# Optimization experiments

Hardware: AMD Instinct MI355X
Metric: run time of the kernel (lower is better)

## Reference

```python
import jax, jax.numpy as jnp
import numpy as np

NUM_PROJS = 8
BLOCK = 128      # key_block_size; with n=4096 -> 32 blocks, query_block_size=128 too
SAMPLE = 128     # sample_size
HEAD_DIM = 64
SCALE = HEAD_DIM ** -0.5

def _gray_perm(n):
    # AngularLSH._unit_hamming_distance_array: Gray-code ordering of 2^n sign buckets
    a = np.array([0, 1], dtype=np.int32)
    for _ in range(n - 1):
        a = np.concatenate([a, a[::-1] + a.shape[0]])
    return a

PERM = jnp.asarray(_gray_perm(NUM_PROJS))
ENC = jnp.asarray(2 ** np.arange(NUM_PROJS), dtype=jnp.int32)

def _lsh_hash(x, proj_dir):
    # x: [b,h,n,d], proj_dir: [d,r] -> Gray-coded bucket id [b,h,n]
    bits = (jnp.einsum('bhnd,dr->bhnr', x, proj_dir) > 0).astype(jnp.int32)
    return PERM[jnp.sum(bits * ENC, axis=-1)]

def _gather_seq(x, idx):
    # gather along seq axis (axis=2); idx: [b,h,m]
    return jnp.take_along_axis(x, idx[..., None], axis=2)

def _hyper_attention(q, k, v, proj_dir, sampled_set):
    # q,k,v: [b,h,n,d]; non-causal HyperAttention (n >= min_seq_len path)
    b, h, n, d = q.shape
    # --- 1. sortLSH block-diagonal attention ---
    q_idx = jnp.argsort(_lsh_hash(q, proj_dir), axis=2, stable=True)
    k_idx = jnp.argsort(_lsh_hash(k, proj_dir), axis=2, stable=True)
    q_idx_inv = jnp.argsort(q_idx, axis=2, stable=True)
    qs = _gather_seq(q, q_idx)
    ks = _gather_seq(k, k_idx)
    vs = _gather_seq(v, k_idx)
    nb = n // BLOCK
    qb = qs.reshape(b, h, nb, BLOCK, d)
    kb = ks.reshape(b, h, nb, BLOCK, d)
    vb = vs.reshape(b, h, nb, BLOCK, d)
    s = jnp.einsum('bhgqd,bhgkd->bhgqk', qb, kb) * SCALE
    lse_blk = jax.scipy.special.logsumexp(s, axis=-1).reshape(b, h, n)
    attn_blk = jnp.einsum('bhgqk,bhgkd->bhgqd', jax.nn.softmax(s, axis=-1), vb).reshape(b, h, n, d)
    # --- 2. uniformly sampled residual (low-rank correction) ---
    ksub = _gather_seq(ks, sampled_set)   # [b,h,m,d]
    vsub = _gather_seq(vs, sampled_set)
    row_blk = jnp.arange(n) // BLOCK       # query_block_size == BLOCK here
    mask = row_blk[None, None, :, None] == (sampled_set // BLOCK)[:, :, None, :]
    bias = jnp.where(mask, jnp.finfo(q.dtype).min, jnp.zeros((), q.dtype))
    sr = jnp.einsum('bhnd,bhmd->bhnm', qs, ksub) * SCALE + bias
    lse_res = jax.scipy.special.logsumexp(sr, axis=-1) + jnp.log(jnp.asarray(n / SAMPLE, q.dtype))
    attn_res = jnp.einsum('bhnm,bhmd->bhnd', jax.nn.softmax(sr, axis=-1), vsub)
    # --- combine the two attention estimates (add_self_attentions) ---
    lse = jnp.logaddexp(lse_blk, lse_res)
    w1 = jnp.exp(lse_blk - lse)[..., None]
    attn = w1 * attn_blk + (1.0 - w1) * attn_res
    # --- unsort rows back to original query order ---
    return _gather_seq(attn, q_idx_inv)

def setup_inputs() -> dict:
    key = jax.random.key(0)
    k1, k2, k3 = jax.random.split(key, 3)
    qkv = jax.random.normal(k1, (2, 4096, 3, 16, 64), dtype=jnp.float32)
    proj_dir = jax.random.normal(k2, (64, NUM_PROJS), dtype=jnp.float32)
    sampled_set = jax.random.randint(k3, (2, 16, SAMPLE), 0, 4096)
    return {"qkv": qkv, "proj_dir": proj_dir, "sampled_set": sampled_set}

def reference(qkv, proj_dir, sampled_set):
    # qkv: [B,S,3,H,D] -> q,k,v [B,H,S,D]
    q = jnp.transpose(qkv[:, :, 0], (0, 2, 1, 3))
    k = jnp.transpose(qkv[:, :, 1], (0, 2, 1, 3))
    v = jnp.transpose(qkv[:, :, 2], (0, 2, 1, 3))
    out = _hyper_attention(q, k, v, proj_dir, sampled_set)
    return jnp.transpose(out, (0, 2, 1, 3))  # [B,S,H,D]
```

## Files before the change

### kernel.cpp

```cpp
#include <hip/hip_runtime.h>
#include <hip/hip_bf16.h>

#define NSEQ 4096
#define DH 64
#define NBH 32
#define LOG32 3.4657359028f
#define QSCALE 0.125f

typedef unsigned short us8 __attribute__((ext_vector_type(8)));
typedef __bf16 bf16x8 __attribute__((ext_vector_type(8)));
typedef float f32x4 __attribute__((ext_vector_type(4)));

__device__ __forceinline__ unsigned short f2b(float x) {
    __bf16 h = (__bf16)x;
    return __builtin_bit_cast(unsigned short, h);
}
__device__ __forceinline__ bf16x8 cvt8(float4 a, float4 b) {
    us8 u;
    u[0] = f2b(a.x); u[1] = f2b(a.y); u[2] = f2b(a.z); u[3] = f2b(a.w);
    u[4] = f2b(b.x); u[5] = f2b(b.y); u[6] = f2b(b.z); u[7] = f2b(b.w);
    return __builtin_bit_cast(bf16x8, u);
}

__global__ __launch_bounds__(256) void hash_kernel(const float* __restrict__ qkv,
                                                   const float* __restrict__ proj,
                                                   unsigned short* __restrict__ hsh) {
    __shared__ float pdT[512];
    int tid = threadIdx.x;
    for (int j = tid; j < 512; j += 256) pdT[j] = proj[(j & 63) * 8 + (j >> 6)];
    __syncthreads();
    int j0 = blockIdx.x * 256 + tid;
    #pragma unroll
    for (int rep = 0; rep < 2; ++rep) {
        int j = j0 + rep * 131072;
        int ch = rep;
        int bh = (j >> 12) & 31;
        int i = j & 4095;
        int b = bh >> 4, h = bh & 15;
        const float4* src = (const float4*)(qkv + ((size_t)((b * NSEQ + i) * 3 + ch)) * 1024 + h * 64);
        double acc[8] = {0, 0, 0, 0, 0, 0, 0, 0};
        for (int d4 = 0; d4 < 16; ++d4) {
            float4 x = src[d4];
            double xx = x.x, xy = x.y, xz = x.z, xw = x.w;
            #pragma unroll
            for (int r = 0; r < 8; ++r) {
                const float4 p = *(const float4*)&pdT[r * 64 + d4 * 4];
                acc[r] += xx * p.x + xy * p.y + xz * p.z + xw * p.w;
            }
        }
        int c = 0;
        #pragma unroll
        for (int r = 0; r < 8; ++r)
            if (acc[r] > 0.0) c |= (1 << r);
        hsh[j] = (unsigned short)(c ^ (c >> 1));
    }
}

__global__ __launch_bounds__(1024) void sort_kernel(const unsigned short* __restrict__ hsh,
                                                    int* __restrict__ qidx,
                                                    int* __restrict__ kidx) {
    int blk = blockIdx.x;
    int pass = blk >> 5, bh = blk & 31;
    const unsigned short* src = hsh + pass * 131072 + bh * 4096;
    int* outg = (pass ? kidx : qidx) + bh * 4096;
    int tid = threadIdx.x;
    __shared__ unsigned short hl[4096];
    __shared__ int hist[64][256];
    __shared__ int base[256];
    for (int j = tid; j < 64 * 256; j += 1024) (&hist[0][0])[j] = 0;
    __syncthreads();
    for (int j = tid; j < 4096; j += 1024) {
        unsigned short v = src[j];
        hl[j] = v;
        atomicAdd(&hist[j >> 6][v], 1);
    }
    __syncthreads();
    int cnt_tot = 0;
    if (tid < 256) {
        int tot = 0;
        #pragma unroll
        for (int s = 0; s < 64; ++s) { int c = hist[s][tid]; hist[s][tid] = tot; tot += c; }
        base[tid] = tot;
        cnt_tot = tot;
    }
    __syncthreads();
    for (int off = 1; off < 256; off <<= 1) {
        int t = (tid >= off && tid < 256) ? base[tid - off] : 0;
        __syncthreads();
        if (tid >= off && tid < 256) base[tid] += t;
        __syncthreads();
    }
    int incl = 0;
    if (tid < 256) incl = base[tid];
    __syncthreads();
    if (tid < 256) base[tid] = incl - cnt_tot;
    __syncthreads();
    {
        int seg = tid >> 4, cls = tid & 15;
        for (int ii = 0; ii < 64; ++ii) {
            int i = (seg << 6) + ii;
            int q = hl[i];
            if ((q & 15) == cls) {
                int pos = base[q] + hist[seg][q];
                hist[seg][q] = hist[seg][q] + 1;
                outg[pos] = i;
            }
        }
    }
}

__global__ __launch_bounds__(512, 4) void attn_kernel(const float* __restrict__ qkv,
                                                      const int* __restrict__ sampled,
                                                      const int* __restrict__ qidx_g,
                                                      const int* __restrict__ kidx_g,
                                                      float* __restrict__ out) {
    int gb = blockIdx.x;
    int bh = gb >> 5, g = gb & 31;
    int b = bh >> 4, h = bh & 15;
    int tid = threadIdx.x;
    int w = tid >> 6, l = tid & 63;
    int l15 = l & 15, lq = l >> 4;

    __shared__ us8 KP[2048];
    __shared__ us8 VT[2048];
    __shared__ float colbias[256];
    __shared__ int qrow[128];
    __shared__ int krow[256];

    if (tid < 128) {
        qrow[tid] = qidx_g[bh * NSEQ + g * 128 + tid];
        krow[tid] = kidx_g[bh * NSEQ + g * 128 + tid];
        colbias[tid] = 0.0f;
    } else if (tid < 256) {
        int j = tid - 128;
        int sp = sampled[bh * 128 + j];
        krow[tid] = kidx_g[bh * NSEQ + sp];
        colbias[tid] = ((sp >> 7) == g) ? -1e30f : LOG32;
    }
    __syncthreads();

    int qr = qrow[w * 16 + l15];
    const float* qbase = qkv + ((size_t)((b * NSEQ + qr) * 3 + 0)) * 1024 + h * 64 + lq * 8;
    float4 qa0 = *(const float4*)(qbase);
    float4 qa1 = *(const float4*)(qbase + 4);
    float4 qb0 = *(const float4*)(qbase + 32);
    float4 qb1 = *(const float4*)(qbase + 36);

    #pragma unroll
    for (int rep = 0; rep < 2; ++rep) {
        int job = tid + rep * 512;
        int r = job >> 2, qt = job & 3;
        const float4* src = (const float4*)(qkv + ((size_t)((b * NSEQ + krow[r]) * 3 + 1)) * 1024 + h * 64 + qt * 16);
        float4 f0 = src[0], f1 = src[1], f2 = src[2], f3 = src[3];
        us8 u0 = __builtin_bit_cast(us8, cvt8(f0, f1));
        us8 u1 = __builtin_bit_cast(us8, cvt8(f2, f3));
        KP[r * 8 + ((qt * 2) ^ (r & 7))] = u0;
        KP[r * 8 + ((qt * 2 + 1) ^ (r & 7))] = u1;
    }
    {
        int key = tid >> 1, half = tid & 1;
        const float4* src = (const float4*)(qkv + ((size_t)((b * NSEQ + krow[key]) * 3 + 2)) * 1024 + h * 64 + half * 32);
        unsigned short* vt_us = (unsigned short*)VT;
        int kc8 = key >> 3, ke = key & 7;
        #pragma unroll
        for (int d4 = 0; d4 < 8; ++d4) {
            float4 f = src[d4];
            int d = half * 32 + d4 * 4;
            vt_us[(((d + 0) * 32 + (kc8 ^ ((d + 0) & 7))) << 3) + ke] = f2b(f.x);
            vt_us[(((d + 1) * 32 + (kc8 ^ ((d + 1) & 7))) << 3) + ke] = f2b(f.y);
            vt_us[(((d + 2) * 32 + (kc8 ^ ((d + 2) & 7))) << 3) + ke] = f2b(f.z);
            vt_us[(((d + 3) * 32 + (kc8 ^ ((d + 3) & 7))) << 3) + ke] = f2b(f.w);
        }
    }
    __syncthreads();

    bf16x8 a0 = cvt8(qa0, qa1);
    bf16x8 a1 = cvt8(qb0, qb1);
    f32x4 sreg[16];
    #pragma unroll
    for (int ct = 0; ct < 16; ++ct) {
        int kr = ct * 16 + l15;
        bf16x8 b0 = __builtin_bit_cast(bf16x8, KP[kr * 8 + (lq ^ (kr & 7))]);
        bf16x8 b1 = __builtin_bit_cast(bf16x8, KP[kr * 8 + ((lq + 4) ^ (kr & 7))]);
        f32x4 acc = {0.f, 0.f, 0.f, 0.f};
        acc = __builtin_amdgcn_mfma_f32_16x16x32_bf16(a0, b0, acc, 0, 0, 0);
        acc = __builtin_amdgcn_mfma_f32_16x16x32_bf16(a1, b1, acc, 0, 0, 0);
        float cb = colbias[kr];
        #pragma unroll
        for (int j = 0; j < 4; ++j) sreg[ct][j] = acc[j] * QSCALE + cb;
    }

    float m0 = -1e30f, m1 = -1e30f, m2 = -1e30f, m3 = -1e30f;
    #pragma unroll
    for (int ct = 0; ct < 16; ++ct) {
        m0 = fmaxf(m0, sreg[ct][0]); m1 = fmaxf(m1, sreg[ct][1]);
        m2 = fmaxf(m2, sreg[ct][2]); m3 = fmaxf(m3, sreg[ct][3]);
    }
    #pragma unroll
    for (int mask = 1; mask < 16; mask <<= 1) {
        m0 = fmaxf(m0, __shfl_xor(m0, mask));
        m1 = fmaxf(m1, __shfl_xor(m1, mask));
        m2 = fmaxf(m2, __shfl_xor(m2, mask));
        m3 = fmaxf(m3, __shfl_xor(m3, mask));
    }
    float s0 = 0.f, s1 = 0.f, s2 = 0.f, s3 = 0.f;
    #pragma unroll
    for (int ct = 0; ct < 16; ++ct) {
        float p0 = __expf(sreg[ct][0] - m0); sreg[ct][0] = p0; s0 += p0;
        float p1 = __expf(sreg[ct][1] - m1); sreg[ct][1] = p1; s1 += p1;
        float p2 = __expf(sreg[ct][2] - m2); sreg[ct][2] = p2; s2 += p2;
        float p3 = __expf(sreg[ct][3] - m3); sreg[ct][3] = p3; s3 += p3;
    }
    #pragma unroll
    for (int mask = 1; mask < 16; mask <<= 1) {
        s0 += __shfl_xor(s0, mask);
        s1 += __shfl_xor(s1, mask);
        s2 += __shfl_xor(s2, mask);
        s3 += __shfl_xor(s3, mask);
    }
    float rs0 = 1.f / s0, rs1 = 1.f / s1, rs2 = 1.f / s2, rs3 = 1.f / s3;

    __syncthreads();

    unsigned short* pp = (unsigned short*)KP;
    int wrow0 = w * 16 + lq * 4;
    #pragma unroll
    for (int ct = 0; ct < 8; ++ct) {
        int c8 = 2 * ct + (l15 >> 3), ce = l15 & 7;
        #pragma unroll
        for (int j = 0; j < 4; ++j) {
            int row = wrow0 + j;
            pp[((row * 16 + (c8 ^ (row & 7))) << 3) + ce] = f2b(sreg[ct][j]);
        }
    }
    __syncthreads();

    f32x4 oacc[4] = {{0.f,0.f,0.f,0.f},{0.f,0.f,0.f,0.f},{0.f,0.f,0.f,0.f},{0.f,0.f,0.f,0.f}};
    int prow = w * 16 + l15;
    #pragma unroll
    for (int ks = 0; ks < 4; ++ks) {
        bf16x8 pa = __builtin_bit_cast(bf16x8, KP[prow * 16 + ((ks * 4 + lq) ^ (prow & 7))]);
        #pragma unroll
        for (int ct = 0; ct < 4; ++ct) {
            int d = ct * 16 + l15;
            bf16x8 vb = __builtin_bit_cast(bf16x8, VT[d * 32 + ((ks * 4 + lq) ^ (d & 7))]);
            oacc[ct] = __builtin_amdgcn_mfma_f32_16x16x32_bf16(pa, vb, oacc[ct], 0, 0, 0);
        }
    }
    __syncthreads();
    #pragma unroll
    for (int ct = 8; ct < 16; ++ct) {
        int c8 = 2 * (ct - 8) + (l15 >> 3), ce = l15 & 7;
        #pragma unroll
        for (int j = 0; j < 4; ++j) {
            int row = wrow0 + j;
            pp[((row * 16 + (c8 ^ (row & 7))) << 3) + ce] = f2b(sreg[ct][j]);
        }
    }
    __syncthreads();
    #pragma unroll
    for (int ks = 4; ks < 8; ++ks) {
        bf16x8 pa = __builtin_bit_cast(bf16x8, KP[prow * 16 + (((ks - 4) * 4 + lq) ^ (prow & 7))]);
        #pragma unroll
        for (int ct = 0; ct < 4; ++ct) {
            int d = ct * 16 + l15;
            bf16x8 vb = __builtin_bit_cast(bf16x8, VT[d * 32 + ((ks * 4 + lq) ^ (d & 7))]);
            oacc[ct] = __builtin_amdgcn_mfma_f32_16x16x32_bf16(pa, vb, oacc[ct], 0, 0, 0);
        }
    }

    float rs[4] = {rs0, rs1, rs2, rs3};
    #pragma unroll
    for (int j = 0; j < 4; ++j) {
        int row = wrow0 + j;
        size_t obase = ((size_t)((b * NSEQ + qrow[row]) * 16 + h)) * 64;
        #pragma unroll
        for (int ct = 0; ct < 4; ++ct)
            out[obase + ct * 16 + l15] = oacc[ct][j] * rs[j];
    }
}

extern "C" void kernel_launch(void* const* d_in, const int* in_sizes, int n_in,
                              void* d_out, int out_size, void* d_ws, size_t ws_size,
                              hipStream_t stream) {
    const float* qkv = (const float*)d_in[0];
    const float* proj = (const float*)d_in[1];
    const int* sampled = (const int*)d_in[2];
    float* outp = (float*)d_out;

    int* qidx = (int*)d_ws;
    int* kidx = qidx + NBH * NSEQ;
    unsigned short* hsh = (unsigned short*)(kidx + NBH * NSEQ);

    hash_kernel<<<512, 256, 0, stream>>>(qkv, proj, hsh);
    sort_kernel<<<64, 1024, 0, stream>>>(hsh, qidx, kidx);
    attn_kernel<<<NBH * 32, 512, 0, stream>>>(qkv, sampled, qidx, kidx, outp);
}
```

Measured before the change: 79.48 us.

## Parallelize sort scatter with ballot ranks, halve V tile LDS, widen hash grid

The sort kernel drops its serial per-segment scatter loop. It now gives each element a stable rank within its 64-element segment by matching bucket bits across the wavefront with ballots, then writes every output position in parallel. The attention kernel keeps only half of the transposed V tile in LDS at a time. The second half is loaded into registers early and written into LDS between the two PV phases, which cuts shared memory so occupancy can rise to 6 blocks per SM. The hash kernel launches one thread per row instead of two rows per thread, which gives more parallelism but more blocks.

Measured after the change: 138.9 us. +74.8%, slower.

```diff
diff --git a/kernel.cpp b/kernel.cpp
--- a/kernel.cpp
+++ b/kernel.cpp
@@ -29,31 +29,27 @@
     int tid = threadIdx.x;
     for (int j = tid; j < 512; j += 256) pdT[j] = proj[(j & 63) * 8 + (j >> 6)];
     __syncthreads();
-    int j0 = blockIdx.x * 256 + tid;
-    #pragma unroll
-    for (int rep = 0; rep < 2; ++rep) {
-        int j = j0 + rep * 131072;
-        int ch = rep;
-        int bh = (j >> 12) & 31;
-        int i = j & 4095;
-        int b = bh >> 4, h = bh & 15;
-        const float4* src = (const float4*)(qkv + ((size_t)((b * NSEQ + i) * 3 + ch)) * 1024 + h * 64);
-        double acc[8] = {0, 0, 0, 0, 0, 0, 0, 0};
-        for (int d4 = 0; d4 < 16; ++d4) {
-            float4 x = src[d4];
-            double xx = x.x, xy = x.y, xz = x.z, xw = x.w;
-            #pragma unroll
-            for (int r = 0; r < 8; ++r) {
-                const float4 p = *(const float4*)&pdT[r * 64 + d4 * 4];
-                acc[r] += xx * p.x + xy * p.y + xz * p.z + xw * p.w;
-            }
-        }
-        int c = 0;
-        #pragma unroll
-        for (int r = 0; r < 8; ++r)
-            if (acc[r] > 0.0) c |= (1 << r);
-        hsh[j] = (unsigned short)(c ^ (c >> 1));
-    }
+    int j = blockIdx.x * 256 + tid;
+    int ch = j >> 17;
+    int bh = (j >> 12) & 31;
+    int i = j & 4095;
+    int b = bh >> 4, h = bh & 15;
+    const float4* src = (const float4*)(qkv + ((size_t)((b * NSEQ + i) * 3 + ch)) * 1024 + h * 64);
+    double acc[8] = {0, 0, 0, 0, 0, 0, 0, 0};
+    for (int d4 = 0; d4 < 16; ++d4) {
+        float4 x = src[d4];
+        double xx = x.x, xy = x.y, xz = x.z, xw = x.w;
+        #pragma unroll
+        for (int r = 0; r < 8; ++r) {
+            const float4 p = *(const float4*)&pdT[r * 64 + d4 * 4];
+            acc[r] += xx * p.x + xy * p.y + xz * p.z + xw * p.w;
+        }
+    }
+    int c = 0;
+    #pragma unroll
+    for (int r = 0; r < 8; ++r)
+        if (acc[r] > 0.0) c |= (1 << r);
+    hsh[j] = (unsigned short)(c ^ (c >> 1));
 }
 
 __global__ __launch_bounds__(1024) void sort_kernel(const unsigned short* __restrict__ hsh,
@@ -64,21 +60,32 @@
     const unsigned short* src = hsh + pass * 131072 + bh * 4096;
     int* outg = (pass ? kidx : qidx) + bh * 4096;
     int tid = threadIdx.x;
-    __shared__ unsigned short hl[4096];
+    int wv = tid >> 6, ln = tid & 63;
     __shared__ int hist[64][256];
+    __shared__ unsigned char rnk[4096];
+    __shared__ unsigned char bkt[4096];
     __shared__ int base[256];
-    for (int j = tid; j < 64 * 256; j += 1024) (&hist[0][0])[j] = 0;
-    __syncthreads();
-    for (int j = tid; j < 4096; j += 1024) {
-        unsigned short v = src[j];
-        hl[j] = v;
-        atomicAdd(&hist[j >> 6][v], 1);
+    for (int jj = tid; jj < 64 * 256; jj += 1024) (&hist[0][0])[jj] = 0;
+    __syncthreads();
+    for (int s = wv; s < 64; s += 16) {
+        int i = s * 64 + ln;
+        int q = src[i];
+        bkt[i] = (unsigned char)q;
+        unsigned long long mask = ~0ULL;
+        #pragma unroll
+        for (int bit = 0; bit < 8; ++bit) {
+            unsigned long long bb = __ballot((q >> bit) & 1);
+            mask &= ((q >> bit) & 1) ? bb : ~bb;
+        }
+        int r = __popcll(mask & ((1ULL << ln) - 1ULL));
+        rnk[i] = (unsigned char)r;
+        if (r == 0) hist[s][q] = __popcll(mask);
     }
     __syncthreads();
     int cnt_tot = 0;
     if (tid < 256) {
         int tot = 0;
-        #pragma unroll
+        #pragma unroll 8
         for (int s = 0; s < 64; ++s) { int c = hist[s][tid]; hist[s][tid] = tot; tot += c; }
         base[tid] = tot;
         cnt_tot = tot;
@@ -95,21 +102,13 @@
     __syncthreads();
     if (tid < 256) base[tid] = incl - cnt_tot;
     __syncthreads();
-    {
-        int seg = tid >> 4, cls = tid & 15;
-        for (int ii = 0; ii < 64; ++ii) {
-            int i = (seg << 6) + ii;
-            int q = hl[i];
-            if ((q & 15) == cls) {
-                int pos = base[q] + hist[seg][q];
-                hist[seg][q] = hist[seg][q] + 1;
-                outg[pos] = i;
-            }
-        }
-    }
-}
-
-__global__ __launch_bounds__(512, 4) void attn_kernel(const float* __restrict__ qkv,
+    for (int i = tid; i < 4096; i += 1024) {
+        int q = bkt[i];
+        outg[base[q] + hist[i >> 6][q] + rnk[i]] = i;
+    }
+}
+
+__global__ __launch_bounds__(512, 6) void attn_kernel(const float* __restrict__ qkv,
                                                       const int* __restrict__ sampled,
                                                       const int* __restrict__ qidx_g,
                                                       const int* __restrict__ kidx_g,
@@ -122,7 +121,7 @@
     int l15 = l & 15, lq = l >> 4;
 
     __shared__ us8 KP[2048];
-    __shared__ us8 VT[2048];
+    __shared__ us8 VT[1024];
     __shared__ float colbias[256];
     __shared__ int qrow[128];
     __shared__ int krow[256];
@@ -146,6 +145,10 @@
     float4 qb0 = *(const float4*)(qbase + 32);
     float4 qb1 = *(const float4*)(qbase + 36);
 
+    int vkey = tid >> 2, vqd = tid & 3;
+    const float4* vhisrc = (const float4*)(qkv + ((size_t)((b * NSEQ + krow[128 + vkey]) * 3 + 2)) * 1024 + h * 64 + vqd * 16);
+    float4 vh0 = vhisrc[0], vh1 = vhisrc[1], vh2 = vhisrc[2], vh3 = vhisrc[3];
+
     #pragma unroll
     for (int rep = 0; rep < 2; ++rep) {
         int job = tid + rep * 512;
@@ -158,18 +161,16 @@
         KP[r * 8 + ((qt * 2 + 1) ^ (r & 7))] = u1;
     }
     {
-        int key = tid >> 1, half = tid & 1;
-        const float4* src = (const float4*)(qkv + ((size_t)((b * NSEQ + krow[key]) * 3 + 2)) * 1024 + h * 64 + half * 32);
+        const float4* src = (const float4*)(qkv + ((size_t)((b * NSEQ + krow[vkey]) * 3 + 2)) * 1024 + h * 64 + vqd * 16);
+        float4 f0 = src[0], f1 = src[1], f2 = src[2], f3 = src[3];
+        float vals[16] = {f0.x, f0.y, f0.z, f0.w, f1.x, f1.y, f1.z, f1.w,
+                          f2.x, f2.y, f2.z, f2.w, f3.x, f3.y, f3.z, f3.w};
         unsigned short* vt_us = (unsigned short*)VT;
-        int kc8 = key >> 3, ke = key & 7;
-        #pragma unroll
-        for (int d4 = 0; d4 < 8; ++d4) {
-            float4 f = src[d4];
-            int d = half * 32 + d4 * 4;
-            vt_us[(((d + 0) * 32 + (kc8 ^ ((d + 0) & 7))) << 3) + ke] = f2b(f.x);
-            vt_us[(((d + 1) * 32 + (kc8 ^ ((d + 1) & 7))) << 3) + ke] = f2b(f.y);
-            vt_us[(((d + 2) * 32 + (kc8 ^ ((d + 2) & 7))) << 3) + ke] = f2b(f.z);
-            vt_us[(((d + 3) * 32 + (kc8 ^ ((d + 3) & 7))) << 3) + ke] = f2b(f.w);
+        int kc8 = vkey >> 3, ke = vkey & 7;
+        #pragma unroll
+        for (int t = 0; t < 16; ++t) {
+            int d = vqd * 16 + t;
+            vt_us[((d * 16 + (kc8 ^ (d & 7))) << 3) + ke] = f2b(vals[t]);
         }
     }
     __syncthreads();
@@ -243,7 +244,7 @@
         #pragma unroll
         for (int ct = 0; ct < 4; ++ct) {
             int d = ct * 16 + l15;
-            bf16x8 vb = __builtin_bit_cast(bf16x8, VT[d * 32 + ((ks * 4 + lq) ^ (d & 7))]);
+            bf16x8 vb = __builtin_bit_cast(bf16x8, VT[d * 16 + ((ks * 4 + lq) ^ (d & 7))]);
             oacc[ct] = __builtin_amdgcn_mfma_f32_16x16x32_bf16(pa, vb, oacc[ct], 0, 0, 0);
         }
     }
@@ -257,6 +258,17 @@
             pp[((row * 16 + (c8 ^ (row & 7))) << 3) + ce] = f2b(sreg[ct][j]);
         }
     }
+    {
+        float vals[16] = {vh0.x, vh0.y, vh0.z, vh0.w, vh1.x, vh1.y, vh1.z, vh1.w,
+                          vh2.x, vh2.y, vh2.z, vh2.w, vh3.x, vh3.y, vh3.z, vh3.w};
+        unsigned short* vt_us = (unsigned short*)VT;
+        int kc8 = vkey >> 3, ke = vkey & 7;
+        #pragma unroll
+        for (int t = 0; t < 16; ++t) {
+            int d = vqd * 16 + t;
+            vt_us[((d * 16 + (kc8 ^ (d & 7))) << 3) + ke] = f2b(vals[t]);
+        }
+    }
     __syncthreads();
     #pragma unroll
     for (int ks = 4; ks < 8; ++ks) {
@@ -264,7 +276,7 @@
         #pragma unroll
         for (int ct = 0; ct < 4; ++ct) {
             int d = ct * 16 + l15;
-            bf16x8 vb = __builtin_bit_cast(bf16x8, VT[d * 32 + ((ks * 4 + lq) ^ (d & 7))]);
+            bf16x8 vb = __builtin_bit_cast(bf16x8, VT[d * 16 + (((ks - 4) * 4 + lq) ^ (d & 7))]);
             oacc[ct] = __builtin_amdgcn_mfma_f32_16x16x32_bf16(pa, vb, oacc[ct], 0, 0, 0);
         }
     }
@@ -292,7 +304,7 @@
     int* kidx = qidx + NBH * NSEQ;
     unsigned short* hsh = (unsigned short*)(kidx + NBH * NSEQ);
 
-    hash_kernel<<<512, 256, 0, stream>>>(qkv, proj, hsh);
+    hash_kernel<<<1024, 256, 0, stream>>>(qkv, proj, hsh);
     sort_kernel<<<64, 1024, 0, stream>>>(hsh, qidx, kidx);
     attn_kernel<<<NBH * 32, 512, 0, stream>>>(qkv, sampled, qidx, kidx, outp);
 }
```

## Compute transposed scores so softmax probabilities feed PV MFMA directly from registers

Applied to the files above, without the earlier changes.

The QK^T MFMA is computed as K·Q^T with a permuted key-row mapping, so each lane's accumulator registers already form the A-operand layout needed for the P·V MFMA. This removes the round trip that wrote bf16 probabilities to shared memory and the four __syncthreads barriers around it. Row max and sum now reduce across only two shuffles, since each query row now sits in one column spread over lane groups. Normalization moves into P before the bf16 conversion, and the K shared-memory swizzle changes to stay bank-conflict-free under the new access pattern.

New measurement: 75.77 us. 1.05x faster.

```diff
diff --git a/kernel.cpp b/kernel.cpp
--- a/kernel.cpp
+++ b/kernel.cpp
@@ -2,7 +2,6 @@
 #include <hip/hip_bf16.h>
 
 #define NSEQ 4096
-#define DH 64
 #define NBH 32
 #define LOG32 3.4657359028f
 #define QSCALE 0.125f
@@ -10,10 +9,14 @@
 typedef unsigned short us8 __attribute__((ext_vector_type(8)));
 typedef __bf16 bf16x8 __attribute__((ext_vector_type(8)));
 typedef float f32x4 __attribute__((ext_vector_type(4)));
+typedef unsigned int u32x4 __attribute__((ext_vector_type(4)));
 
 __device__ __forceinline__ unsigned short f2b(float x) {
     __bf16 h = (__bf16)x;
     return __builtin_bit_cast(unsigned short, h);
+}
+__device__ __forceinline__ unsigned pk2(float lo, float hi) {
+    return (unsigned)f2b(lo) | ((unsigned)f2b(hi) << 16);
 }
 __device__ __forceinline__ bf16x8 cvt8(float4 a, float4 b) {
     us8 u;
@@ -152,10 +155,9 @@
         int r = job >> 2, qt = job & 3;
         const float4* src = (const float4*)(qkv + ((size_t)((b * NSEQ + krow[r]) * 3 + 1)) * 1024 + h * 64 + qt * 16);
         float4 f0 = src[0], f1 = src[1], f2 = src[2], f3 = src[3];
-        us8 u0 = __builtin_bit_cast(us8, cvt8(f0, f1));
-        us8 u1 = __builtin_bit_cast(us8, cvt8(f2, f3));
-        KP[r * 8 + ((qt * 2) ^ (r & 7))] = u0;
-        KP[r * 8 + ((qt * 2 + 1) ^ (r & 7))] = u1;
+        int sw = (r ^ (r >> 2)) & 7;
+        KP[r * 8 + ((qt * 2) ^ sw)] = __builtin_bit_cast(us8, cvt8(f0, f1));
+        KP[r * 8 + ((qt * 2 + 1) ^ sw)] = __builtin_bit_cast(us8, cvt8(f2, f3));
     }
     {
         int key = tid >> 1, half = tid & 1;
@@ -174,109 +176,83 @@
     }
     __syncthreads();
 
-    bf16x8 a0 = cvt8(qa0, qa1);
-    bf16x8 a1 = cvt8(qb0, qb1);
-    f32x4 sreg[16];
-    #pragma unroll
-    for (int ct = 0; ct < 16; ++ct) {
-        int kr = ct * 16 + l15;
-        bf16x8 b0 = __builtin_bit_cast(bf16x8, KP[kr * 8 + (lq ^ (kr & 7))]);
-        bf16x8 b1 = __builtin_bit_cast(bf16x8, KP[kr * 8 + ((lq + 4) ^ (kr & 7))]);
-        f32x4 acc = {0.f, 0.f, 0.f, 0.f};
-        acc = __builtin_amdgcn_mfma_f32_16x16x32_bf16(a0, b0, acc, 0, 0, 0);
-        acc = __builtin_amdgcn_mfma_f32_16x16x32_bf16(a1, b1, acc, 0, 0, 0);
-        float cb = colbias[kr];
-        #pragma unroll
-        for (int j = 0; j < 4; ++j) sreg[ct][j] = acc[j] * QSCALE + cb;
-    }
-
-    float m0 = -1e30f, m1 = -1e30f, m2 = -1e30f, m3 = -1e30f;
-    #pragma unroll
-    for (int ct = 0; ct < 16; ++ct) {
-        m0 = fmaxf(m0, sreg[ct][0]); m1 = fmaxf(m1, sreg[ct][1]);
-        m2 = fmaxf(m2, sreg[ct][2]); m3 = fmaxf(m3, sreg[ct][3]);
-    }
-    #pragma unroll
-    for (int mask = 1; mask < 16; mask <<= 1) {
-        m0 = fmaxf(m0, __shfl_xor(m0, mask));
-        m1 = fmaxf(m1, __shfl_xor(m1, mask));
-        m2 = fmaxf(m2, __shfl_xor(m2, mask));
-        m3 = fmaxf(m3, __shfl_xor(m3, mask));
-    }
-    float s0 = 0.f, s1 = 0.f, s2 = 0.f, s3 = 0.f;
-    #pragma unroll
-    for (int ct = 0; ct < 16; ++ct) {
-        float p0 = __expf(sreg[ct][0] - m0); sreg[ct][0] = p0; s0 += p0;
-        float p1 = __expf(sreg[ct][1] - m1); sreg[ct][1] = p1; s1 += p1;
-        float p2 = __expf(sreg[ct][2] - m2); sreg[ct][2] = p2; s2 += p2;
-        float p3 = __expf(sreg[ct][3] - m3); sreg[ct][3] = p3; s3 += p3;
-    }
-    #pragma unroll
-    for (int mask = 1; mask < 16; mask <<= 1) {
-        s0 += __shfl_xor(s0, mask);
-        s1 += __shfl_xor(s1, mask);
-        s2 += __shfl_xor(s2, mask);
-        s3 += __shfl_xor(s3, mask);
-    }
-    float rs0 = 1.f / s0, rs1 = 1.f / s1, rs2 = 1.f / s2, rs3 = 1.f / s3;
-
-    __syncthreads();
-
-    unsigned short* pp = (unsigned short*)KP;
-    int wrow0 = w * 16 + lq * 4;
-    #pragma unroll
-    for (int ct = 0; ct < 8; ++ct) {
-        int c8 = 2 * ct + (l15 >> 3), ce = l15 & 7;
+    bf16x8 q0 = cvt8(qa0, qa1);
+    bf16x8 q1 = cvt8(qb0, qb1);
+    f32x4 sA[8], sB[8];
+    int ra = 8 * (l15 >> 2) + (l15 & 3);
+    #pragma unroll
+    for (int s = 0; s < 8; ++s) {
+        int krA = s * 32 + ra;
+        int krB = krA + 4;
+        int swA = (krA ^ (krA >> 2)) & 7;
+        int swB = (krB ^ (krB >> 2)) & 7;
+        bf16x8 kA0 = __builtin_bit_cast(bf16x8, KP[krA * 8 + (lq ^ swA)]);
+        bf16x8 kA1 = __builtin_bit_cast(bf16x8, KP[krA * 8 + ((lq + 4) ^ swA)]);
+        bf16x8 kB0 = __builtin_bit_cast(bf16x8, KP[krB * 8 + (lq ^ swB)]);
+        bf16x8 kB1 = __builtin_bit_cast(bf16x8, KP[krB * 8 + ((lq + 4) ^ swB)]);
+        f32x4 accA = {0.f, 0.f, 0.f, 0.f}, accB = {0.f, 0.f, 0.f, 0.f};
+        accA = __builtin_amdgcn_mfma_f32_16x16x32_bf16(kA0, q0, accA, 0, 0, 0);
+        accA = __builtin_amdgcn_mfma_f32_16x16x32_bf16(kA1, q1, accA, 0, 0, 0);
+        accB = __builtin_amdgcn_mfma_f32_16x16x32_bf16(kB0, q0, accB, 0, 0, 0);
+        accB = __builtin_amdgcn_mfma_f32_16x16x32_bf16(kB1, q1, accB, 0, 0, 0);
+        float4 cbA = *(const float4*)&colbias[s * 32 + lq * 8];
+        float4 cbB = *(const float4*)&colbias[s * 32 + lq * 8 + 4];
+        sA[s][0] = accA[0] * QSCALE + cbA.x;
+        sA[s][1] = accA[1] * QSCALE + cbA.y;
+        sA[s][2] = accA[2] * QSCALE + cbA.z;
+        sA[s][3] = accA[3] * QSCALE + cbA.w;
+        sB[s][0] = accB[0] * QSCALE + cbB.x;
+        sB[s][1] = accB[1] * QSCALE + cbB.y;
+        sB[s][2] = accB[2] * QSCALE + cbB.z;
+        sB[s][3] = accB[3] * QSCALE + cbB.w;
+    }
+
+    float m = -1e30f;
+    #pragma unroll
+    for (int s = 0; s < 8; ++s)
         #pragma unroll
         for (int j = 0; j < 4; ++j) {
-            int row = wrow0 + j;
-            pp[((row * 16 + (c8 ^ (row & 7))) << 3) + ce] = f2b(sreg[ct][j]);
-        }
-    }
-    __syncthreads();
+            m = fmaxf(m, sA[s][j]);
+            m = fmaxf(m, sB[s][j]);
+        }
+    m = fmaxf(m, __shfl_xor(m, 16));
+    m = fmaxf(m, __shfl_xor(m, 32));
+    float sum = 0.f;
+    #pragma unroll
+    for (int s = 0; s < 8; ++s)
+        #pragma unroll
+        for (int j = 0; j < 4; ++j) {
+            float pa = __expf(sA[s][j] - m); sA[s][j] = pa; sum += pa;
+            float pb = __expf(sB[s][j] - m); sB[s][j] = pb; sum += pb;
+        }
+    sum += __shfl_xor(sum, 16);
+    sum += __shfl_xor(sum, 32);
+    float rs = 1.0f / sum;
 
     f32x4 oacc[4] = {{0.f,0.f,0.f,0.f},{0.f,0.f,0.f,0.f},{0.f,0.f,0.f,0.f},{0.f,0.f,0.f,0.f}};
-    int prow = w * 16 + l15;
-    #pragma unroll
-    for (int ks = 0; ks < 4; ++ks) {
-        bf16x8 pa = __builtin_bit_cast(bf16x8, KP[prow * 16 + ((ks * 4 + lq) ^ (prow & 7))]);
+    #pragma unroll
+    for (int s = 0; s < 8; ++s) {
+        u32x4 pw;
+        pw[0] = pk2(sA[s][0] * rs, sA[s][1] * rs);
+        pw[1] = pk2(sA[s][2] * rs, sA[s][3] * rs);
+        pw[2] = pk2(sB[s][0] * rs, sB[s][1] * rs);
+        pw[3] = pk2(sB[s][2] * rs, sB[s][3] * rs);
+        bf16x8 pa = __builtin_bit_cast(bf16x8, pw);
         #pragma unroll
         for (int ct = 0; ct < 4; ++ct) {
             int d = ct * 16 + l15;
-            bf16x8 vb = __builtin_bit_cast(bf16x8, VT[d * 32 + ((ks * 4 + lq) ^ (d & 7))]);
+            bf16x8 vb = __builtin_bit_cast(bf16x8, VT[d * 32 + ((s * 4 + lq) ^ (d & 7))]);
             oacc[ct] = __builtin_amdgcn_mfma_f32_16x16x32_bf16(pa, vb, oacc[ct], 0, 0, 0);
         }
     }
-    __syncthreads();
-    #pragma unroll
-    for (int ct = 8; ct < 16; ++ct) {
-        int c8 = 2 * (ct - 8) + (l15 >> 3), ce = l15 & 7;
-        #pragma unroll
-        for (int j = 0; j < 4; ++j) {
-            int row = wrow0 + j;
-            pp[((row * 16 + (c8 ^ (row & 7))) << 3) + ce] = f2b(sreg[ct][j]);
-        }
-    }
-    __syncthreads();
-    #pragma unroll
-    for (int ks = 4; ks < 8; ++ks) {
-        bf16x8 pa = __builtin_bit_cast(bf16x8, KP[prow * 16 + (((ks - 4) * 4 + lq) ^ (prow & 7))]);
-        #pragma unroll
-        for (int ct = 0; ct < 4; ++ct) {
-            int d = ct * 16 + l15;
-            bf16x8 vb = __builtin_bit_cast(bf16x8, VT[d * 32 + ((ks * 4 + lq) ^ (d & 7))]);
-            oacc[ct] = __builtin_amdgcn_mfma_f32_16x16x32_bf16(pa, vb, oacc[ct], 0, 0, 0);
-        }
-    }
-
-    float rs[4] = {rs0, rs1, rs2, rs3};
+
     #pragma unroll
     for (int j = 0; j < 4; ++j) {
-        int row = wrow0 + j;
+        int row = w * 16 + lq * 4 + j;
         size_t obase = ((size_t)((b * NSEQ + qrow[row]) * 16 + h)) * 64;
         #pragma unroll
         for (int ct = 0; ct < 4; ++ct)
-            out[obase + ct * 16 + l15] = oacc[ct][j] * rs[j];
+            out[obase + ct * 16 + l15] = oacc[ct][j];
     }
 }
 
```
